# Optimization experiments

Measured on AMD Instinct MI355X. Metric: run time of the kernel, lower is better.

Reference implementation:

```python
import jax, jax.numpy as jnp
import numpy as np

B, N, IN_C, HID_C, OUT_C = 8, 2048, 128, 256, 32


def setup_inputs() -> dict:
    key = jax.random.key(0)
    ks = jax.random.split(key, 8)
    s1 = 1.0 / np.sqrt(IN_C)
    s2 = 1.0 / np.sqrt(HID_C)
    return {
        "x": jax.random.normal(ks[0], (B, N, IN_C), dtype=jnp.float32),
        "A": jax.random.randint(ks[1], (B, N, N), 0, 2, dtype=jnp.int32),
        "W1_l": jax.random.normal(ks[2], (IN_C, HID_C), dtype=jnp.float32) * s1,
        "W1_r": jax.random.normal(ks[3], (IN_C, HID_C), dtype=jnp.float32) * s1,
        "b1": jnp.zeros((HID_C,), dtype=jnp.float32),
        "W2_l": jax.random.normal(ks[4], (HID_C, OUT_C), dtype=jnp.float32) * s2,
        "W2_r": jax.random.normal(ks[5], (HID_C, OUT_C), dtype=jnp.float32) * s2,
        "b2": jnp.zeros((OUT_C,), dtype=jnp.float32),
    }


def _mean_agg(mask, deg_inv, h):
    # edge (i, j) means source i -> target j (PyG source_to_target flow):
    # agg[b, j] = mean over i with A[b, i, j] != 0 of h[b, i]
    return jnp.einsum("bij,bid->bjd", mask, h) * deg_inv


def reference(x, A, W1_l, W1_r, b1, W2_l, W2_r, b2):
    mask = (A != 0).astype(x.dtype)            # [B, N, N]
    deg = jnp.sum(mask, axis=1)                # in-degree per target node, [B, N]
    deg_inv = (1.0 / jnp.maximum(deg, 1.0))[..., None]  # isolated nodes -> 0 agg

    # SAGEConv 1: lin_l(mean_agg(x)) + lin_r(x) + bias, then ReLU
    # (dropout p=0.2 is inactive in eval mode)
    h = _mean_agg(mask, deg_inv, x) @ W1_l + x @ W1_r + b1
    h = jax.nn.relu(h)

    # SAGEConv 2
    out = _mean_agg(mask, deg_inv, h) @ W2_l + h @ W2_r + b2  # [B, N, OUT_C]
    return (jax.nn.log_softmax(out, axis=-1), out)
```

## Files before the change

kernel.cpp:

```cpp
#include <hip/hip_runtime.h>


#define B_   8
#define N_   2048
#define INC  128
#define HID  256
#define OUTC 32

typedef __attribute__((ext_vector_type(8))) __bf16 bf16x8;
typedef __attribute__((ext_vector_type(4))) float f32x4;
typedef __attribute__((ext_vector_type(4))) unsigned int u32x4;
typedef __attribute__((ext_vector_type(2))) unsigned int u32x2;

__device__ __forceinline__ unsigned short f2bf(float f) {
  unsigned int u = __float_as_uint(f);
  u += 0x7FFFu + ((u >> 16) & 1u);
  return (unsigned short)(u >> 16);
}

__device__ __forceinline__ f32x4 mfma16(bf16x8 a, bf16x8 b, f32x4 c) {
  return __builtin_amdgcn_mfma_f32_16x16x32_bf16(a, b, c, 0, 0, 0);
}

__device__ __forceinline__ bf16x8 ones_frag() {
  union { unsigned short u[8]; bf16x8 v; } o;
#pragma unroll
  for (int i = 0; i < 8; i++) o.u[i] = 0x3F80;
  return o.v;
}

__device__ __forceinline__ void lut_init(u32x2* lut, int t) {
  if (t < 16) {
    unsigned int w0 = (t & 1 ? 0x3F80u : 0u) | (t & 2 ? 0x3F800000u : 0u);
    unsigned int w1 = (t & 4 ? 0x3F80u : 0u) | (t & 8 ? 0x3F800000u : 0u);
    u32x2 e = {w0, w1};
    lut[t] = e;
  }
}

__device__ __forceinline__ bf16x8 expand8(const u32x2* lut, unsigned int bval) {
  union { u32x2 u2[2]; bf16x8 v; } af;
  af.u2[0] = lut[bval & 15u];
  af.u2[1] = lut[bval >> 4];
  return af.v;
}

__global__ __launch_bounds__(256, 8) void k_prep(
    const int* __restrict__ A, const float* __restrict__ x,
    const float* __restrict__ W1l, const float* __restrict__ W1r,
    const float* __restrict__ W2l, const float* __restrict__ W2r,
    unsigned int* __restrict__ bits, unsigned short* __restrict__ xT,
    unsigned short* __restrict__ acat1,
    unsigned short* __restrict__ W1cT, unsigned short* __restrict__ W2cT) {
  __shared__ unsigned short xls[128 * 72];
  const int bx = blockIdx.x, t = threadIdx.x;
  if (bx < 2048) {
    const int w = t >> 6, l = t & 63;
    const int gw = bx * 4 + w;
    const int b = gw >> 10;
    const int it = (gw >> 5) & 31, jt = gw & 31;
    const int i0 = it * 64, j0 = jt * 64;
    const int* Ap = A + ((size_t)(b * N_) + i0) * N_ + j0 + l;
    unsigned long long col = 0;
#pragma unroll 8
    for (int r = 0; r < 64; r++) {
      int a = Ap[(size_t)r * N_];
      unsigned long long m = __ballot(a != 0);
      col |= ((m >> l) & 1ull) << r;
    }
    *reinterpret_cast<unsigned long long*>(
        bits + ((size_t)(b * N_) + j0 + l) * 64 + (i0 >> 5)) = col;
  } else if (bx < 2304) {
    const int bb = bx - 2048;
    const int b = bb >> 5, it = bb & 31, i0 = it * 64;
    const int dq = (t & 31) * 4;
    const int irow = t >> 5;
#pragma unroll
    for (int s = 0; s < 8; s++) {
      int il = s * 8 + irow;
      int i = i0 + il;
      f32x4 v = *reinterpret_cast<const f32x4*>(x + ((size_t)(b * N_ + i)) * INC + dq);
      unsigned int p0 = f2bf(v[0]) | ((unsigned int)f2bf(v[1]) << 16);
      unsigned int p1 = f2bf(v[2]) | ((unsigned int)f2bf(v[3]) << 16);
      u32x2 pk = {p0, p1};
      *reinterpret_cast<u32x2*>(acat1 + ((size_t)(b * N_ + i)) * HID + 128 + dq) = pk;
      xls[(dq + 0) * 72 + il] = f2bf(v[0]);
      xls[(dq + 1) * 72 + il] = f2bf(v[1]);
      xls[(dq + 2) * 72 + il] = f2bf(v[2]);
      xls[(dq + 3) * 72 + il] = f2bf(v[3]);
    }
    __syncthreads();
    const int d = t >> 1, half = t & 1;
    const u32x4* src = reinterpret_cast<const u32x4*>(&xls[d * 72 + half * 32]);
    u32x4* dst = reinterpret_cast<u32x4*>(xT + ((size_t)(b * INC + d)) * N_ + i0 + half * 32);
#pragma unroll
    for (int q = 0; q < 4; q++) dst[q] = src[q];
  } else if (bx < 2368) {
    int base = (bx - 2304) * 1024 + t * 4;
#pragma unroll
    for (int q = 0; q < 4; q++) {
      int id = base + q;
      int e = id >> 8, k = id & 255;
      float v = (k < 128) ? W1l[k * 256 + e] : W1r[(k - 128) * 256 + e];
      W1cT[id] = f2bf(v);
    }
  } else {
    int base = (bx - 2368) * 1024 + t * 4;
#pragma unroll
    for (int q = 0; q < 4; q++) {
      int id = base + q;
      int n = id >> 8, k = id & 255;
      float v = (n < 32) ? W2l[k * 32 + n] : W2r[k * 32 + (n - 32)];
      W2cT[id] = f2bf(v);
    }
  }
}

__global__ __launch_bounds__(256, 2) void k_agg1(
    const unsigned int* __restrict__ bits, const unsigned short* __restrict__ xT,
    unsigned short* __restrict__ acat1, float* __restrict__ deg_inv) {
  __shared__ u32x2 lut[16];
  __shared__ __align__(16) float part[3][2][8][64][4];
  __shared__ __align__(16) float pdeg[3][2][16][4];
  const int t = threadIdx.x;
  const int w = t >> 6, l = t & 63, lr = l & 15, lq = l >> 4;
  lut_init(lut, t);
  __syncthreads();
  const int b = blockIdx.y, j0 = blockIdx.x * 32;
  const unsigned int* bp0 = bits + ((size_t)(b * N_ + j0 + lr)) * 64 + w * 16;
  const unsigned int* bp1 = bp0 + (size_t)16 * 64;
  const unsigned short* xb = xT + (size_t)b * INC * N_ + w * 512;

  const f32x4 zero = {0.f, 0.f, 0.f, 0.f};
  f32x4 acc[2][8];
#pragma unroll
  for (int jt = 0; jt < 2; jt++)
#pragma unroll
    for (int ds = 0; ds < 8; ds++) acc[jt][ds] = zero;
  f32x4 dacc[2] = {zero, zero};
  const bf16x8 onesf = ones_frag();

  for (int s = 0; s < 16; s++) {
    bf16x8 af0 = expand8(lut, (bp0[s] >> (lq * 8)) & 0xFFu);
    bf16x8 af1 = expand8(lut, (bp1[s] >> (lq * 8)) & 0xFFu);
    dacc[0] = mfma16(af0, onesf, dacc[0]);
    dacc[1] = mfma16(af1, onesf, dacc[1]);
#pragma unroll
    for (int ds = 0; ds < 8; ds++) {
      bf16x8 bfr = *reinterpret_cast<const bf16x8*>(
          xb + ((size_t)(ds * 16 + lr)) * N_ + s * 32 + lq * 8);
      acc[0][ds] = mfma16(af0, bfr, acc[0][ds]);
      acc[1][ds] = mfma16(af1, bfr, acc[1][ds]);
    }
  }

  if (w > 0) {
#pragma unroll
    for (int jt = 0; jt < 2; jt++) {
#pragma unroll
      for (int ds = 0; ds < 8; ds++)
        *reinterpret_cast<f32x4*>(&part[w - 1][jt][ds][l][0]) = acc[jt][ds];
      if (lr == 0) *reinterpret_cast<f32x4*>(&pdeg[w - 1][jt][lq][0]) = dacc[jt];
    }
  }
  __syncthreads();
  if (w != 0) return;

  unsigned short* ag = acat1 + ((size_t)(b * N_ + j0)) * HID;
#pragma unroll
  for (int jt = 0; jt < 2; jt++) {
    float dinv[4];
#pragma unroll
    for (int r = 0; r < 4; r++) {
      float deg = dacc[jt][r] + pdeg[0][jt][lq][r] + pdeg[1][jt][lq][r] +
                  pdeg[2][jt][lq][r];
      dinv[r] = 1.0f / fmaxf(deg, 1.0f);
    }
    if (lr == 0) {
#pragma unroll
      for (int r = 0; r < 4; r++)
        deg_inv[b * N_ + j0 + jt * 16 + lq * 4 + r] = dinv[r];
    }
#pragma unroll
    for (int ds = 0; ds < 8; ds++) {
      f32x4 v0 = *reinterpret_cast<f32x4*>(&part[0][jt][ds][l][0]);
      f32x4 v1 = *reinterpret_cast<f32x4*>(&part[1][jt][ds][l][0]);
      f32x4 v2 = *reinterpret_cast<f32x4*>(&part[2][jt][ds][l][0]);
#pragma unroll
      for (int r = 0; r < 4; r++)
        ag[(size_t)(jt * 16 + lq * 4 + r) * HID + ds * 16 + lr] =
            f2bf((acc[jt][ds][r] + v0[r] + v1[r] + v2[r]) * dinv[r]);
    }
  }
}

__global__ __launch_bounds__(256, 2) void k_dense2(
    const unsigned short* __restrict__ acat1, const unsigned short* __restrict__ W1cT,
    const unsigned short* __restrict__ W2cT, const float* __restrict__ b1,
    const float* __restrict__ b2, unsigned short* __restrict__ hlT,
    float* __restrict__ hr) {
  __shared__ __align__(16) unsigned short hs[32 * 264];
  const int t = threadIdx.x;
  const int w = t >> 6, l = t & 63, lr = l & 15, lq = l >> 4;
  const int b = blockIdx.y, j0 = blockIdx.x * 32;
  const int e0 = w * 64;

  const f32x4 zero = {0.f, 0.f, 0.f, 0.f};
  f32x4 acc[2][4];
#pragma unroll
  for (int jt = 0; jt < 2; jt++)
#pragma unroll
    for (int es = 0; es < 4; es++) acc[jt][es] = zero;

#pragma unroll
  for (int ks = 0; ks < 8; ks++) {
    bf16x8 af0 = *reinterpret_cast<const bf16x8*>(
        acat1 + ((size_t)(b * N_ + j0 + lr)) * HID + ks * 32 + lq * 8);
    bf16x8 af1 = *reinterpret_cast<const bf16x8*>(
        acat1 + ((size_t)(b * N_ + j0 + 16 + lr)) * HID + ks * 32 + lq * 8);
#pragma unroll
    for (int es = 0; es < 4; es++) {
      bf16x8 bfr = *reinterpret_cast<const bf16x8*>(
          W1cT + ((size_t)(e0 + es * 16 + lr)) * HID + ks * 32 + lq * 8);
      acc[0][es] = mfma16(af0, bfr, acc[0][es]);
      acc[1][es] = mfma16(af1, bfr, acc[1][es]);
    }
  }
#pragma unroll
  for (int jt = 0; jt < 2; jt++)
#pragma unroll
    for (int es = 0; es < 4; es++) {
      int e = e0 + es * 16 + lr;
      float bias = b1[e];
#pragma unroll
      for (int r = 0; r < 4; r++)
        hs[(jt * 16 + lq * 4 + r) * 264 + e] = f2bf(fmaxf(acc[jt][es][r] + bias, 0.0f));
    }
  __syncthreads();

  const int jt = w & 1, nh = w >> 1;
  f32x4 a2[2] = {zero, zero};
#pragma unroll
  for (int ks = 0; ks < 8; ks++) {
    bf16x8 af = *reinterpret_cast<const bf16x8*>(&hs[(jt * 16 + lr) * 264 + ks * 32 + lq * 8]);
#pragma unroll
    for (int ns = 0; ns < 2; ns++) {
      bf16x8 bfr = *reinterpret_cast<const bf16x8*>(
          W2cT + ((size_t)(nh * 32 + ns * 16 + lr)) * HID + ks * 32 + lq * 8);
      a2[ns] = mfma16(af, bfr, a2[ns]);
    }
  }
  if (nh == 0) {
#pragma unroll
    for (int ns = 0; ns < 2; ns++) {
      int c = ns * 16 + lr;
      unsigned int p0 = f2bf(a2[ns][0]) | ((unsigned int)f2bf(a2[ns][1]) << 16);
      unsigned int p1 = f2bf(a2[ns][2]) | ((unsigned int)f2bf(a2[ns][3]) << 16);
      u32x2 pk = {p0, p1};
      *reinterpret_cast<u32x2*>(
          hlT + ((size_t)(b * 32 + c)) * N_ + j0 + jt * 16 + lq * 4) = pk;
    }
  } else {
#pragma unroll
    for (int ns = 0; ns < 2; ns++) {
      int c = ns * 16 + lr;
      float bias = b2[c];
#pragma unroll
      for (int r = 0; r < 4; r++)
        hr[((size_t)(b * N_ + j0 + jt * 16 + lq * 4 + r)) * OUTC + c] = a2[ns][r] + bias;
    }
  }
}

__global__ __launch_bounds__(256, 2) void k_agg2out(
    const unsigned int* __restrict__ bits, const unsigned short* __restrict__ hlT,
    const float* __restrict__ deg_inv, const float* __restrict__ hr,
    float* __restrict__ out) {
  __shared__ u32x2 lut[16];
  __shared__ __align__(16) float part[4][2][2][64][4];
  const int t = threadIdx.x;
  const int w = t >> 6, l = t & 63, lr = l & 15, lq = l >> 4;
  lut_init(lut, t);
  __syncthreads();
  const int b = blockIdx.y, j0 = blockIdx.x * 32;
  const unsigned int* bp0 = bits + ((size_t)(b * N_ + j0 + lr)) * 64 + w * 16;
  const unsigned int* bp1 = bp0 + (size_t)16 * 64;
  const unsigned short* hb = hlT + (size_t)b * 32 * N_ + w * 512;

  const f32x4 zero = {0.f, 0.f, 0.f, 0.f};
  f32x4 acc[2][2] = {{zero, zero}, {zero, zero}};

  for (int s = 0; s < 16; s++) {
    bf16x8 af0 = expand8(lut, (bp0[s] >> (lq * 8)) & 0xFFu);
    bf16x8 af1 = expand8(lut, (bp1[s] >> (lq * 8)) & 0xFFu);
#pragma unroll
    for (int cs = 0; cs < 2; cs++) {
      bf16x8 bfr = *reinterpret_cast<const bf16x8*>(
          hb + ((size_t)(cs * 16 + lr)) * N_ + s * 32 + lq * 8);
      acc[0][cs] = mfma16(af0, bfr, acc[0][cs]);
      acc[1][cs] = mfma16(af1, bfr, acc[1][cs]);
    }
  }
#pragma unroll
  for (int jt = 0; jt < 2; jt++)
#pragma unroll
    for (int cs = 0; cs < 2; cs++)
      *reinterpret_cast<f32x4*>(&part[w][jt][cs][l][0]) = acc[jt][cs];
  __syncthreads();
  if (w >= 2) return;

  const int jt = w;
  const size_t SZ = (size_t)B_ * N_ * OUTC;
#pragma unroll
  for (int r = 0; r < 4; r++) {
    int j = j0 + jt * 16 + lq * 4 + r;
    float dv = deg_inv[b * N_ + j];
    size_t base = ((size_t)(b * N_ + j)) * OUTC;
    float v0 = (part[0][jt][0][l][r] + part[1][jt][0][l][r] +
                part[2][jt][0][l][r] + part[3][jt][0][l][r]) * dv + hr[base + lr];
    float v1 = (part[0][jt][1][l][r] + part[1][jt][1][l][r] +
                part[2][jt][1][l][r] + part[3][jt][1][l][r]) * dv + hr[base + 16 + lr];
    float m = fmaxf(v0, v1);
#pragma unroll
    for (int d = 1; d < 16; d <<= 1) m = fmaxf(m, __shfl_xor(m, d, 64));
    float s = __expf(v0 - m) + __expf(v1 - m);
#pragma unroll
    for (int d = 1; d < 16; d <<= 1) s += __shfl_xor(s, d, 64);
    float ls = m + __logf(s);
    out[base + lr] = v0 - ls;
    out[base + 16 + lr] = v1 - ls;
    out[SZ + base + lr] = v0;
    out[SZ + base + 16 + lr] = v1;
  }
}

extern "C" void kernel_launch(void* const* d_in, const int* in_sizes, int n_in,
                              void* d_out, int out_size, void* d_ws, size_t ws_size,
                              hipStream_t stream) {
  (void)in_sizes; (void)n_in; (void)out_size; (void)ws_size;
  const float* x   = (const float*)d_in[0];
  const int*   A   = (const int*)d_in[1];
  const float* W1l = (const float*)d_in[2];
  const float* W1r = (const float*)d_in[3];
  const float* b1  = (const float*)d_in[4];
  const float* W2l = (const float*)d_in[5];
  const float* W2r = (const float*)d_in[6];
  const float* b2  = (const float*)d_in[7];
  float* out = (float*)d_out;

  char* ws = (char*)d_ws;
  unsigned short* W1cT    = (unsigned short*)(ws + 0);
  unsigned short* W2cT    = (unsigned short*)(ws + 131072);
  float*          deg_inv = (float*)(ws + 163840);
  unsigned int*   bits    = (unsigned int*)(ws + 229376);
  unsigned short* xT      = (unsigned short*)(ws + 4423680);
  unsigned short* hlT     = (unsigned short*)(ws + 4423680);
  float*          hr      = (float*)(ws + 5472256);
  unsigned short* acat1   = (unsigned short*)(ws + 8617984);

  k_prep   <<<dim3(2384),  dim3(256), 0, stream>>>(A, x, W1l, W1r, W2l, W2r,
                                                   bits, xT, acat1, W1cT, W2cT);
  k_agg1   <<<dim3(64, 8), dim3(256), 0, stream>>>(bits, xT, acat1, deg_inv);
  k_dense2 <<<dim3(64, 8), dim3(256), 0, stream>>>(acat1, W1cT, W2cT, b1, b2,
                                                   hlT, hr);
  k_agg2out<<<dim3(64, 8), dim3(256), 0, stream>>>(bits, hlT, deg_inv, hr, out);
}
```

Before: 287.8 us.

## Fuse first aggregation with dense layers and interleave batches across blocks

Merges the layer-1 aggregation kernel and the dense-projection kernel into one kernel. The aggregated features and the bf16 copy of x are kept in shared memory instead of making a round trip through a global acat buffer. The cross-wave reduction is now split across all four waves instead of being done by wave 0 alone. Grid indexing is also changed so consecutive blocks cycle through the batch index, which spreads work across batches. In exchange the fused kernel uses more shared memory per block, which may lower occupancy.

```diff
diff --git a/kernel.cpp b/kernel.cpp
--- a/kernel.cpp
+++ b/kernel.cpp
@@ -50,15 +50,15 @@
     const float* __restrict__ W1l, const float* __restrict__ W1r,
     const float* __restrict__ W2l, const float* __restrict__ W2r,
     unsigned int* __restrict__ bits, unsigned short* __restrict__ xT,
-    unsigned short* __restrict__ acat1,
+    unsigned short* __restrict__ xcat,
     unsigned short* __restrict__ W1cT, unsigned short* __restrict__ W2cT) {
   __shared__ unsigned short xls[128 * 72];
   const int bx = blockIdx.x, t = threadIdx.x;
   if (bx < 2048) {
     const int w = t >> 6, l = t & 63;
-    const int gw = bx * 4 + w;
-    const int b = gw >> 10;
-    const int it = (gw >> 5) & 31, jt = gw & 31;
+    const int b = bx & 7, tile4 = bx >> 3;
+    const int gw2 = tile4 * 4 + w;
+    const int it = gw2 >> 5, jt = gw2 & 31;
     const int i0 = it * 64, j0 = jt * 64;
     const int* Ap = A + ((size_t)(b * N_) + i0) * N_ + j0 + l;
     unsigned long long col = 0;
@@ -72,7 +72,8 @@
         bits + ((size_t)(b * N_) + j0 + l) * 64 + (i0 >> 5)) = col;
   } else if (bx < 2304) {
     const int bb = bx - 2048;
-    const int b = bb >> 5, it = bb & 31, i0 = it * 64;
+    const int b = bb & 7, it = bb >> 3;
+    const int i0 = it * 64;
     const int dq = (t & 31) * 4;
     const int irow = t >> 5;
 #pragma unroll
@@ -83,7 +84,7 @@
       unsigned int p0 = f2bf(v[0]) | ((unsigned int)f2bf(v[1]) << 16);
       unsigned int p1 = f2bf(v[2]) | ((unsigned int)f2bf(v[3]) << 16);
       u32x2 pk = {p0, p1};
-      *reinterpret_cast<u32x2*>(acat1 + ((size_t)(b * N_ + i)) * HID + 128 + dq) = pk;
+      *reinterpret_cast<u32x2*>(xcat + ((size_t)(b * N_ + i)) * INC + dq) = pk;
       xls[(dq + 0) * 72 + il] = f2bf(v[0]);
       xls[(dq + 1) * 72 + il] = f2bf(v[1]);
       xls[(dq + 2) * 72 + il] = f2bf(v[2]);
@@ -116,17 +117,35 @@
   }
 }
 
-__global__ __launch_bounds__(256, 2) void k_agg1(
+__global__ __launch_bounds__(256, 2) void k_fused1(
     const unsigned int* __restrict__ bits, const unsigned short* __restrict__ xT,
-    unsigned short* __restrict__ acat1, float* __restrict__ deg_inv) {
+    const unsigned short* __restrict__ xcat,
+    const unsigned short* __restrict__ W1cT, const unsigned short* __restrict__ W2cT,
+    const float* __restrict__ b1, const float* __restrict__ b2,
+    unsigned short* __restrict__ hlT, float* __restrict__ hr,
+    float* __restrict__ deg_inv) {
   __shared__ u32x2 lut[16];
-  __shared__ __align__(16) float part[3][2][8][64][4];
-  __shared__ __align__(16) float pdeg[3][2][16][4];
+  __shared__ __align__(16) float pdeg[4][2][16][4];
+  __shared__ __align__(16) unsigned short acat_s[32 * 264];
+  union SU {
+    float part[4][6][2][64][4];
+    unsigned short hs[32 * 264];
+  };
+  __shared__ __align__(16) SU su;
+
   const int t = threadIdx.x;
   const int w = t >> 6, l = t & 63, lr = l & 15, lq = l >> 4;
   lut_init(lut, t);
-  __syncthreads();
-  const int b = blockIdx.y, j0 = blockIdx.x * 32;
+
+  const int b = blockIdx.x & 7, j0 = (blockIdx.x >> 3) * 32;
+
+  const int xr = t >> 3, xs = t & 7;
+  const unsigned short* xp = xcat + ((size_t)(b * N_ + j0 + xr)) * INC + xs * 16;
+  u32x4 xpart0 = *reinterpret_cast<const u32x4*>(xp);
+  u32x4 xpart1 = *reinterpret_cast<const u32x4*>(xp + 8);
+
+  __syncthreads();
+
   const unsigned int* bp0 = bits + ((size_t)(b * N_ + j0 + lr)) * 64 + w * 16;
   const unsigned int* bp1 = bp0 + (size_t)16 * 64;
   const unsigned short* xb = xT + (size_t)b * INC * N_ + w * 512;
@@ -154,78 +173,79 @@
     }
   }
 
-  if (w > 0) {
+#pragma unroll
+  for (int ds = 0; ds < 8; ds++) {
+    if ((ds >> 1) != w) {
+      int dsi = (ds < 2 * w) ? ds : ds - 2;
+#pragma unroll
+      for (int jt = 0; jt < 2; jt++)
+        *reinterpret_cast<f32x4*>(&su.part[w][dsi][jt][l][0]) = acc[jt][ds];
+    }
+  }
+  if (lr == 0) {
+#pragma unroll
+    for (int jt = 0; jt < 2; jt++)
+      *reinterpret_cast<f32x4*>(&pdeg[w][jt][lq][0]) = dacc[jt];
+  }
+  *reinterpret_cast<u32x4*>(&acat_s[xr * 264 + 128 + xs * 16]) = xpart0;
+  *reinterpret_cast<u32x4*>(&acat_s[xr * 264 + 128 + xs * 16 + 8]) = xpart1;
+  __syncthreads();
+
+  float dinv2[2][4];
+#pragma unroll
+  for (int jt = 0; jt < 2; jt++)
+#pragma unroll
+    for (int r = 0; r < 4; r++) {
+      float deg = pdeg[0][jt][lq][r] + pdeg[1][jt][lq][r] +
+                  pdeg[2][jt][lq][r] + pdeg[3][jt][lq][r];
+      dinv2[jt][r] = 1.0f / fmaxf(deg, 1.0f);
+    }
+  if (w < 2 && lr == 0) {
+#pragma unroll
+    for (int r = 0; r < 4; r++)
+      deg_inv[b * N_ + j0 + w * 16 + lq * 4 + r] = dinv2[w][r];
+  }
+#pragma unroll
+  for (int dd = 0; dd < 2; dd++) {
+    int ds = 2 * w + dd;
 #pragma unroll
     for (int jt = 0; jt < 2; jt++) {
-#pragma unroll
-      for (int ds = 0; ds < 8; ds++)
-        *reinterpret_cast<f32x4*>(&part[w - 1][jt][ds][l][0]) = acc[jt][ds];
-      if (lr == 0) *reinterpret_cast<f32x4*>(&pdeg[w - 1][jt][lq][0]) = dacc[jt];
-    }
-  }
-  __syncthreads();
-  if (w != 0) return;
-
-  unsigned short* ag = acat1 + ((size_t)(b * N_ + j0)) * HID;
-#pragma unroll
-  for (int jt = 0; jt < 2; jt++) {
-    float dinv[4];
-#pragma unroll
-    for (int r = 0; r < 4; r++) {
-      float deg = dacc[jt][r] + pdeg[0][jt][lq][r] + pdeg[1][jt][lq][r] +
-                  pdeg[2][jt][lq][r];
-      dinv[r] = 1.0f / fmaxf(deg, 1.0f);
-    }
-    if (lr == 0) {
+      f32x4 sum = acc[jt][ds];
+#pragma unroll
+      for (int src = 0; src < 4; src++) {
+        if (src != w) {
+          int dsi = (ds < 2 * src) ? ds : ds - 2;
+          f32x4 p = *reinterpret_cast<f32x4*>(&su.part[src][dsi][jt][l][0]);
+          sum += p;
+        }
+      }
 #pragma unroll
       for (int r = 0; r < 4; r++)
-        deg_inv[b * N_ + j0 + jt * 16 + lq * 4 + r] = dinv[r];
-    }
-#pragma unroll
-    for (int ds = 0; ds < 8; ds++) {
-      f32x4 v0 = *reinterpret_cast<f32x4*>(&part[0][jt][ds][l][0]);
-      f32x4 v1 = *reinterpret_cast<f32x4*>(&part[1][jt][ds][l][0]);
-      f32x4 v2 = *reinterpret_cast<f32x4*>(&part[2][jt][ds][l][0]);
-#pragma unroll
-      for (int r = 0; r < 4; r++)
-        ag[(size_t)(jt * 16 + lq * 4 + r) * HID + ds * 16 + lr] =
-            f2bf((acc[jt][ds][r] + v0[r] + v1[r] + v2[r]) * dinv[r]);
-    }
-  }
-}
-
-__global__ __launch_bounds__(256, 2) void k_dense2(
-    const unsigned short* __restrict__ acat1, const unsigned short* __restrict__ W1cT,
-    const unsigned short* __restrict__ W2cT, const float* __restrict__ b1,
-    const float* __restrict__ b2, unsigned short* __restrict__ hlT,
-    float* __restrict__ hr) {
-  __shared__ __align__(16) unsigned short hs[32 * 264];
-  const int t = threadIdx.x;
-  const int w = t >> 6, l = t & 63, lr = l & 15, lq = l >> 4;
-  const int b = blockIdx.y, j0 = blockIdx.x * 32;
+        acat_s[(jt * 16 + lq * 4 + r) * 264 + ds * 16 + lr] =
+            f2bf(sum[r] * dinv2[jt][r]);
+    }
+  }
+  __syncthreads();
+
+  f32x4 acc2[2][4];
+#pragma unroll
+  for (int jt = 0; jt < 2; jt++)
+#pragma unroll
+    for (int es = 0; es < 4; es++) acc2[jt][es] = zero;
   const int e0 = w * 64;
-
-  const f32x4 zero = {0.f, 0.f, 0.f, 0.f};
-  f32x4 acc[2][4];
-#pragma unroll
-  for (int jt = 0; jt < 2; jt++)
-#pragma unroll
-    for (int es = 0; es < 4; es++) acc[jt][es] = zero;
-
 #pragma unroll
   for (int ks = 0; ks < 8; ks++) {
-    bf16x8 af0 = *reinterpret_cast<const bf16x8*>(
-        acat1 + ((size_t)(b * N_ + j0 + lr)) * HID + ks * 32 + lq * 8);
-    bf16x8 af1 = *reinterpret_cast<const bf16x8*>(
-        acat1 + ((size_t)(b * N_ + j0 + 16 + lr)) * HID + ks * 32 + lq * 8);
+    bf16x8 af0 = *reinterpret_cast<const bf16x8*>(&acat_s[lr * 264 + ks * 32 + lq * 8]);
+    bf16x8 af1 = *reinterpret_cast<const bf16x8*>(&acat_s[(16 + lr) * 264 + ks * 32 + lq * 8]);
 #pragma unroll
     for (int es = 0; es < 4; es++) {
       bf16x8 bfr = *reinterpret_cast<const bf16x8*>(
           W1cT + ((size_t)(e0 + es * 16 + lr)) * HID + ks * 32 + lq * 8);
-      acc[0][es] = mfma16(af0, bfr, acc[0][es]);
-      acc[1][es] = mfma16(af1, bfr, acc[1][es]);
-    }
-  }
+      acc2[0][es] = mfma16(af0, bfr, acc2[0][es]);
+      acc2[1][es] = mfma16(af1, bfr, acc2[1][es]);
+    }
+  }
+  __syncthreads();
 #pragma unroll
   for (int jt = 0; jt < 2; jt++)
 #pragma unroll
@@ -234,7 +254,8 @@
       float bias = b1[e];
 #pragma unroll
       for (int r = 0; r < 4; r++)
-        hs[(jt * 16 + lq * 4 + r) * 264 + e] = f2bf(fmaxf(acc[jt][es][r] + bias, 0.0f));
+        su.hs[(jt * 16 + lq * 4 + r) * 264 + e] =
+            f2bf(fmaxf(acc2[jt][es][r] + bias, 0.0f));
     }
   __syncthreads();
 
@@ -242,7 +263,8 @@
   f32x4 a2[2] = {zero, zero};
 #pragma unroll
   for (int ks = 0; ks < 8; ks++) {
-    bf16x8 af = *reinterpret_cast<const bf16x8*>(&hs[(jt * 16 + lr) * 264 + ks * 32 + lq * 8]);
+    bf16x8 af = *reinterpret_cast<const bf16x8*>(
+        &su.hs[(jt * 16 + lr) * 264 + ks * 32 + lq * 8]);
 #pragma unroll
     for (int ns = 0; ns < 2; ns++) {
       bf16x8 bfr = *reinterpret_cast<const bf16x8*>(
@@ -282,7 +304,7 @@
   const int w = t >> 6, l = t & 63, lr = l & 15, lq = l >> 4;
   lut_init(lut, t);
   __syncthreads();
-  const int b = blockIdx.y, j0 = blockIdx.x * 32;
+  const int b = blockIdx.x & 7, j0 = (blockIdx.x >> 3) * 32;
   const unsigned int* bp0 = bits + ((size_t)(b * N_ + j0 + lr)) * 64 + w * 16;
   const unsigned int* bp1 = bp0 + (size_t)16 * 64;
   const unsigned short* hb = hlT + (size_t)b * 32 * N_ + w * 512;
@@ -354,14 +376,13 @@
   float*          deg_inv = (float*)(ws + 163840);
   unsigned int*   bits    = (unsigned int*)(ws + 229376);
   unsigned short* xT      = (unsigned short*)(ws + 4423680);
-  unsigned short* hlT     = (unsigned short*)(ws + 4423680);
-  float*          hr      = (float*)(ws + 5472256);
-  unsigned short* acat1   = (unsigned short*)(ws + 8617984);
-
-  k_prep   <<<dim3(2384),  dim3(256), 0, stream>>>(A, x, W1l, W1r, W2l, W2r,
-                                                   bits, xT, acat1, W1cT, W2cT);
-  k_agg1   <<<dim3(64, 8), dim3(256), 0, stream>>>(bits, xT, acat1, deg_inv);
-  k_dense2 <<<dim3(64, 8), dim3(256), 0, stream>>>(acat1, W1cT, W2cT, b1, b2,
-                                                   hlT, hr);
-  k_agg2out<<<dim3(64, 8), dim3(256), 0, stream>>>(bits, hlT, deg_inv, hr, out);
-}
+  unsigned short* xcat    = (unsigned short*)(ws + 8617984);
+  unsigned short* hlT     = (unsigned short*)(ws + 12812288);
+  float*          hr      = (float*)(ws + 13860864);
+
+  k_prep   <<<dim3(2384), dim3(256), 0, stream>>>(A, x, W1l, W1r, W2l, W2r,
+                                                  bits, xT, xcat, W1cT, W2cT);
+  k_fused1 <<<dim3(512),  dim3(256), 0, stream>>>(bits, xT, xcat, W1cT, W2cT,
+                                                  b1, b2, hlT, hr, deg_inv);
+  k_agg2out<<<dim3(512),  dim3(256), 0, stream>>>(bits, hlT, deg_inv, hr, out);
+}
```

Result: no change. 284.3 us (-1.2%).
